# Kernel tuning notes

Hardware: AMD Instinct MI355X
Metric: run time of the kernel (lower is better)

The kernel has to match this reference:

```python
import jax, jax.numpy as jnp
import numpy as np

MOMENTUM = 0.9
EPS_MASK = 1e-6   # torch clamp(min=1e-6) on mask sum
EPS_NORM = 1e-12  # torch F.normalize eps

def _l2norm(x):
    n = jnp.linalg.norm(x, axis=-1, keepdims=True)
    return x / jnp.maximum(n, EPS_NORM)

def setup_inputs() -> dict:
    key = jax.random.key(0)
    k1, k2, k3, k4, k5 = jax.random.split(key, 5)
    num_users, num_proto, embd_dim = 50000, 16, 128
    B, S = 8192, 50
    return {
        "user_prototypes": jax.random.normal(k1, (num_users, num_proto, embd_dim), jnp.float32),
        "shared_prototypes": jax.random.normal(k2, (1, num_proto, embd_dim), jnp.float32),
        "interaction_count": jax.random.uniform(k3, (num_users,), jnp.float32),
        "features": jax.random.normal(k4, (B, S, embd_dim), jnp.float32),
        "success_mask": jax.random.uniform(k5, (B, S), jnp.float32),
        "user_idx": jnp.arange(B, dtype=jnp.int64) if jax.config.jax_enable_x64 else jnp.arange(B, dtype=jnp.int32),
    }

def reference(user_prototypes, shared_prototypes, interaction_count, features, success_mask, user_idx):
    # --- gather ---
    current = user_prototypes[user_idx]                    # [B, P, D]
    ic = interaction_count[user_idx]                       # [B]
    m = jnp.clip(MOMENTUM + ic / 1000.0, MOMENTUM, 0.99)[:, None, None]
    # --- masked reduction over history (features dim==3 branch, mask dim==2) ---
    mask = success_mask[..., None]                         # [B, S, 1]
    upd = (features * mask).sum(axis=1) / jnp.maximum(mask.sum(axis=1), EPS_MASK)  # [B, D]
    upd = _l2norm(upd)                                     # F.normalize(dim=-1)
    upd = jnp.broadcast_to(upd[:, None, :], current.shape) # expand to [B, P, D]
    # --- momentum blend + scatter write ---
    new_batch = m * current + (1.0 - m) * upd
    new_user_prototypes = user_prototypes.at[user_idx].set(new_batch)
    # --- shared prototype update ---
    shared_upd = _l2norm(upd.mean(axis=0))                 # [P, D]
    new_shared = MOMENTUM * shared_prototypes + (1.0 - MOMENTUM) * shared_upd[None]
    # --- interaction count increment ---
    new_ic = interaction_count.at[user_idx].add(1.0)
    return new_user_prototypes, new_shared, new_ic
```

## Files before the change

kernel.cpp:

```cpp
#include <hip/hip_runtime.h>

#define NB 8192
#define NS 50
#define ND 128
#define NP 16
#define NU 50000
#define NRED 128

typedef float f4v __attribute__((ext_vector_type(4)));

__global__ void k_scatter_map(const int* __restrict__ user_idx, int* __restrict__ map) {
    int b = blockIdx.x * blockDim.x + threadIdx.x;
    if (b < NB) map[user_idx[b]] = b;
}

__global__ __launch_bounds__(256) void k_big(
    const float* __restrict__ proto,
    const float* __restrict__ ic,
    const float* __restrict__ features,
    const float* __restrict__ mask,
    const int* __restrict__ map,
    const int* __restrict__ user_idx,
    float* __restrict__ out_proto,
    float* __restrict__ out_ic,
    float* __restrict__ upd)
{
    int u = blockIdx.x;
    int t = threadIdx.x;

    int b = map[u];
    bool mapped = (b >= 0) && (b < NB);
    if (mapped) mapped = (user_idx[b] == u);

    const f4v* proto4 = (const f4v*)proto;
    f4v* out4 = (f4v*)out_proto;
    size_t base = (size_t)u * (NP * ND / 4);

    if (!mapped) {
        f4v v0 = __builtin_nontemporal_load(&proto4[base + t]);
        f4v v1 = __builtin_nontemporal_load(&proto4[base + t + 256]);
        __builtin_nontemporal_store(v0, &out4[base + t]);
        __builtin_nontemporal_store(v1, &out4[base + t + 256]);
        if (t == 0) out_ic[u] = ic[u];
        return;
    }

    __shared__ float smask[NS];
    __shared__ f4v   part[8][32];
    __shared__ f4v   updv[32];

    if (t < NS) smask[t] = mask[(size_t)b * NS + t];
    __syncthreads();

    int q = t & 31;
    int g = t >> 5;
    const f4v* f4 = (const f4v*)features + (size_t)b * (NS * ND / 4);
    f4v acc = {0.f, 0.f, 0.f, 0.f};
    for (int s = g; s < NS; s += 8) {
        float w = smask[s];
        f4v v = __builtin_nontemporal_load(&f4[s * 32 + q]);
        acc += v * w;
    }
    part[g][q] = acc;
    __syncthreads();

    if (t < 32) {
        float msum = 0.f;
#pragma unroll
        for (int s = 0; s < NS; ++s) msum += smask[s];

        f4v a = part[0][t];
#pragma unroll
        for (int g2 = 1; g2 < 8; ++g2) a += part[g2][t];

        a *= (1.0f / fmaxf(msum, 1e-6f));

        float d2 = a.x * a.x + a.y * a.y + a.z * a.z + a.w * a.w;
#pragma unroll
        for (int mm = 16; mm >= 1; mm >>= 1) d2 += __shfl_xor(d2, mm, 64);
        a *= (1.0f / fmaxf(sqrtf(d2), 1e-12f));

        updv[t] = a;
        ((f4v*)upd)[(size_t)b * 32 + t] = a;
    }
    __syncthreads();

    float icv = ic[u];
    float m = fminf(fmaxf(0.9f + icv * 0.001f, 0.9f), 0.99f);
    float om = 1.0f - m;
    if (t == 0) out_ic[u] = icv + 1.0f;

#pragma unroll
    for (int rep = 0; rep < 2; ++rep) {
        int idx = t + rep * 256;
        f4v v = __builtin_nontemporal_load(&proto4[base + idx]);
        f4v uu = updv[idx & 31];
        v = m * v + om * uu;
        __builtin_nontemporal_store(v, &out4[base + idx]);
    }
}

__global__ void k_colsum(const float* __restrict__ upd, float* __restrict__ part) {
    int blk = blockIdx.x;
    int t = threadIdx.x;
    int d = t & 127;
    int h = t >> 7;

    const int rows = NB / NRED;
    int r0 = blk * rows;

    float s = 0.f;
    for (int r = r0 + h; r < r0 + rows; r += 2)
        s += upd[(size_t)r * ND + d];

    __shared__ float red[2][ND];
    red[h][d] = s;
    __syncthreads();
    if (h == 0)
        part[(size_t)blk * ND + d] = red[0][d] + red[1][d];
}

__global__ void k_shared_final(const float* __restrict__ part,
                               const float* __restrict__ shared_in,
                               float* __restrict__ shared_out) {
    int d = threadIdx.x;

    float tot = 0.f;
#pragma unroll
    for (int j = 0; j < NRED; ++j) tot += part[(size_t)j * ND + d];
    float mean = tot / (float)NB;

    __shared__ float red[ND];
    red[d] = mean * mean;
    __syncthreads();
    for (int off = 64; off > 0; off >>= 1) {
        if (d < off) red[d] += red[d + off];
        __syncthreads();
    }
    float inv = 1.0f / fmaxf(sqrtf(red[0]), 1e-12f);
    float su = mean * inv;

#pragma unroll
    for (int p = 0; p < NP; ++p)
        shared_out[p * ND + d] = 0.9f * shared_in[p * ND + d] + 0.1f * su;
}

extern "C" void kernel_launch(void* const* d_in, const int* in_sizes, int n_in,
                              void* d_out, int out_size, void* d_ws, size_t ws_size,
                              hipStream_t stream) {
    const float* user_prototypes   = (const float*)d_in[0];
    const float* shared_prototypes = (const float*)d_in[1];
    const float* interaction_count = (const float*)d_in[2];
    const float* features          = (const float*)d_in[3];
    const float* success_mask      = (const float*)d_in[4];
    const int*   user_idx          = (const int*)d_in[5];

    float* out_proto  = (float*)d_out;
    float* out_shared = out_proto + (size_t)NU * NP * ND;
    float* out_ic     = out_shared + NP * ND;

    int*   map  = (int*)d_ws;
    float* upd  = (float*)((char*)d_ws + 200704);
    float* part = upd + (size_t)NB * ND;

    k_scatter_map<<<(NB + 255) / 256, 256, 0, stream>>>(user_idx, map);

    k_big<<<NU, 256, 0, stream>>>(user_prototypes, interaction_count,
                                  features, success_mask, map, user_idx,
                                  out_proto, out_ic, upd);

    k_colsum<<<NRED, 256, 0, stream>>>(upd, part);
    k_shared_final<<<1, ND, 0, stream>>>(part, shared_prototypes, out_shared);
}
```

Measured before the change: 189.8 us.

## Split fused kernel into separate update-reduction and uniform blend/copy kernels

The single kernel that handled both the masked feature reduction for mapped users and the prototype copy/blend for every user is split in two. A new kernel computes the normalized update vectors for all batch rows, and a second, uniform kernel streams every user's prototypes and applies the blend when mapped. This removes divergence and load imbalance between heavy and light blocks in the big grid and lets the blend kernel have fixed, small per-block work. The cost is an extra launch and a round trip of the update vectors through global memory.

```diff
diff --git a/kernel.cpp b/kernel.cpp
--- a/kernel.cpp
+++ b/kernel.cpp
@@ -14,40 +14,16 @@
     if (b < NB) map[user_idx[b]] = b;
 }
 
-__global__ __launch_bounds__(256) void k_big(
-    const float* __restrict__ proto,
-    const float* __restrict__ ic,
+__global__ __launch_bounds__(256) void k_upd(
     const float* __restrict__ features,
     const float* __restrict__ mask,
-    const int* __restrict__ map,
-    const int* __restrict__ user_idx,
-    float* __restrict__ out_proto,
-    float* __restrict__ out_ic,
     float* __restrict__ upd)
 {
-    int u = blockIdx.x;
+    int b = blockIdx.x;
     int t = threadIdx.x;
-
-    int b = map[u];
-    bool mapped = (b >= 0) && (b < NB);
-    if (mapped) mapped = (user_idx[b] == u);
-
-    const f4v* proto4 = (const f4v*)proto;
-    f4v* out4 = (f4v*)out_proto;
-    size_t base = (size_t)u * (NP * ND / 4);
-
-    if (!mapped) {
-        f4v v0 = __builtin_nontemporal_load(&proto4[base + t]);
-        f4v v1 = __builtin_nontemporal_load(&proto4[base + t + 256]);
-        __builtin_nontemporal_store(v0, &out4[base + t]);
-        __builtin_nontemporal_store(v1, &out4[base + t + 256]);
-        if (t == 0) out_ic[u] = ic[u];
-        return;
-    }
 
     __shared__ float smask[NS];
     __shared__ f4v   part[8][32];
-    __shared__ f4v   updv[32];
 
     if (t < NS) smask[t] = mask[(size_t)b * NS + t];
     __syncthreads();
@@ -80,24 +56,47 @@
         for (int mm = 16; mm >= 1; mm >>= 1) d2 += __shfl_xor(d2, mm, 64);
         a *= (1.0f / fmaxf(sqrtf(d2), 1e-12f));
 
-        updv[t] = a;
         ((f4v*)upd)[(size_t)b * 32 + t] = a;
     }
-    __syncthreads();
+}
 
-    float icv = ic[u];
-    float m = fminf(fmaxf(0.9f + icv * 0.001f, 0.9f), 0.99f);
-    float om = 1.0f - m;
-    if (t == 0) out_ic[u] = icv + 1.0f;
+__global__ __launch_bounds__(256) void k_blend(
+    const float* __restrict__ proto,
+    const float* __restrict__ ic,
+    const int* __restrict__ map,
+    const int* __restrict__ user_idx,
+    const float* __restrict__ upd,
+    float* __restrict__ out_proto,
+    float* __restrict__ out_ic)
+{
+    int u = blockIdx.x;
+    int t = threadIdx.x;
 
-#pragma unroll
-    for (int rep = 0; rep < 2; ++rep) {
-        int idx = t + rep * 256;
-        f4v v = __builtin_nontemporal_load(&proto4[base + idx]);
-        f4v uu = updv[idx & 31];
-        v = m * v + om * uu;
-        __builtin_nontemporal_store(v, &out4[base + idx]);
+    int b = map[u];
+    bool mapped = (b >= 0) && (b < NB);
+    if (mapped) mapped = (user_idx[b] == u);
+
+    const f4v* proto4 = (const f4v*)proto;
+    f4v* out4 = (f4v*)out_proto;
+    size_t base = (size_t)u * (NP * ND / 4);
+
+    f4v v0 = __builtin_nontemporal_load(&proto4[base + t]);
+    f4v v1 = __builtin_nontemporal_load(&proto4[base + t + 256]);
+
+    if (mapped) {
+        float icv = ic[u];
+        float m = fminf(fmaxf(0.9f + icv * 0.001f, 0.9f), 0.99f);
+        float om = 1.0f - m;
+        f4v uu = ((const f4v*)upd)[(size_t)b * 32 + (t & 31)];
+        v0 = m * v0 + om * uu;
+        v1 = m * v1 + om * uu;
+        if (t == 0) out_ic[u] = icv + 1.0f;
+    } else {
+        if (t == 0) out_ic[u] = ic[u];
     }
+
+    __builtin_nontemporal_store(v0, &out4[base + t]);
+    __builtin_nontemporal_store(v1, &out4[base + t + 256]);
 }
 
 __global__ void k_colsum(const float* __restrict__ upd, float* __restrict__ part) {
@@ -163,11 +162,12 @@
     float* upd  = (float*)((char*)d_ws + 200704);
     float* part = upd + (size_t)NB * ND;
 
+    k_upd<<<NB, 256, 0, stream>>>(features, success_mask, upd);
+
     k_scatter_map<<<(NB + 255) / 256, 256, 0, stream>>>(user_idx, map);
 
-    k_big<<<NU, 256, 0, stream>>>(user_prototypes, interaction_count,
-                                  features, success_mask, map, user_idx,
-                                  out_proto, out_ic, upd);
+    k_blend<<<NU, 256, 0, stream>>>(user_prototypes, interaction_count,
+                                    map, user_idx, upd, out_proto, out_ic);
 
     k_colsum<<<NRED, 256, 0, stream>>>(upd, part);
     k_shared_final<<<1, ND, 0, stream>>>(part, shared_prototypes, out_shared);
```

New measurement: 181.4 us. -4.4%, faster.
